# Kernel optimization log

Hardware: AMD Instinct MI355X
Metric: run time of the kernel (lower is better)

## Reference

```python
import jax, jax.numpy as jnp
import numpy as np
import math


def setup_inputs() -> dict:
    key = jax.random.key(0)
    ks = jax.random.split(key, 10)
    B, N, C, heads = 16, 1024, 256, 8
    nW = 4
    ANGLE_BINS = 5
    inner = C  # dim_head*heads == dim
    return {
        "x": jax.random.normal(ks[0], (B, N, C), jnp.float32),
        "mask": jax.random.normal(ks[1], (nW, N, N), jnp.float32),
        "affine_matrix": jax.random.normal(ks[2], (B, 2, 3), jnp.float32),
        "Wq": jax.random.normal(ks[3], (C, inner), jnp.float32) * (C ** -0.5),
        "bq": jnp.zeros((inner,), jnp.float32),
        "Wkv": jax.random.normal(ks[4], (C, 2 * inner), jnp.float32) * (C ** -0.5),
        "bkv": jnp.zeros((2 * inner,), jnp.float32),
        "Wp": jax.random.normal(ks[5], (C, C), jnp.float32) * (C ** -0.5),
        "bp": jnp.zeros((C,), jnp.float32),
        "angle_table": jnp.ones((ANGLE_BINS, heads), jnp.float32),
        "H": 32,
        "W": 32,
    }


def reference(x, mask, affine_matrix, Wq, bq, Wkv, bkv, Wp, bp, angle_table, H, W):
    B, N, C = x.shape
    heads = angle_table.shape[1]
    hd = C // heads
    scale = hd ** -0.5

    # qkv projections (torch Linear -> x @ W + b with W stored as (in, out))
    q = (x @ Wq + bq).reshape(B, N, heads, hd).transpose(0, 2, 1, 3)      # (B,h,N,d)
    kv = (x @ Wkv + bkv).reshape(B, N, 2, heads, hd).transpose(2, 0, 3, 1, 4)
    k, v = kv[0], kv[1]                                                    # (B,h,N,d)

    attn = jnp.einsum('bhqd,bhkd->bhqk', q * scale, k)                     # (B,h,N,N)

    # angle bias: per-query multiplicative bias in (1,2)
    grid_y, grid_x = jnp.meshgrid(jnp.arange(H), jnp.arange(W), indexing='ij')
    coords = jnp.stack([grid_x.reshape(-1), grid_y.reshape(-1)], -1).astype(jnp.float32)  # (N,2)
    center = jnp.array([W / 2.0, H / 2.0], jnp.float32)
    ego = jnp.einsum('bij,j->bi', affine_matrix[:, :2, :2], center) + affine_matrix[:, :2, 2]  # (B,2)
    rel = coords[None, :, :] - ego[:, None, :]                             # (B,N,2)
    ang = jnp.arctan2(rel[..., 1], rel[..., 0])
    bins = (((ang + math.pi) / (2.0 * math.pi)) * (angle_table.shape[0] - 1)).astype(jnp.int32)
    bias = 1.0 + jax.nn.sigmoid(angle_table[bins])                         # (B,N,h)
    attn = attn * bias.transpose(0, 2, 1)[..., None]                       # broadcast over keys

    # additive window mask then softmax
    nW = mask.shape[0]
    attn = attn.reshape(B // nW, nW, heads, N, N) + mask[None, :, None]
    attn = jax.nn.softmax(attn.reshape(B, heads, N, N), axis=-1)

    out = jnp.einsum('bhqk,bhkd->bhqd', attn, v).transpose(0, 2, 1, 3).reshape(B, N, C)
    return out @ Wp + bp
```

## Files before the change

### kernel.cpp

```cpp
#include <hip/hip_runtime.h>
#include <hip/hip_bf16.h>
#include <math.h>

#define BB 16
#define NTOK 1024
#define CDIM 256
#define HEADS 8
#define HD 32
#define LOG2E 1.4426950408889634f
#define PSHIFT 18.0f

typedef __attribute__((ext_vector_type(8))) _Float16 half8;
typedef __attribute__((ext_vector_type(8))) unsigned short u16x8;
typedef __attribute__((ext_vector_type(4))) unsigned int u32x4;
typedef __attribute__((ext_vector_type(2))) unsigned int u32x2;
typedef __attribute__((ext_vector_type(4))) float f32x4;

__device__ __forceinline__ unsigned short f2h(float f) {
  _Float16 h = (_Float16)f;
  return __builtin_bit_cast(unsigned short, h);
}
__device__ __forceinline__ half8 ldh8(const unsigned short* p) {
  return *reinterpret_cast<const half8*>(p);
}
__device__ __forceinline__ void gl_lds16(const unsigned short* g,
                                         unsigned short* l) {
  __builtin_amdgcn_global_load_lds(
      (const __attribute__((address_space(1))) unsigned int*)g,
      (__attribute__((address_space(3))) unsigned int*)l, 16, 0, 0);
}

__global__ __launch_bounds__(256) void cvt_x(const float* __restrict__ X,
                                             unsigned short* __restrict__ x16) {
  size_t base = ((size_t)blockIdx.x * 256 + threadIdx.x) * 8;
  float4 a = *(const float4*)(X + base);
  float4 b = *(const float4*)(X + base + 4);
  u16x8 o = {f2h(a.x), f2h(a.y), f2h(a.z), f2h(a.w),
             f2h(b.x), f2h(b.y), f2h(b.z), f2h(b.w)};
  *(u16x8*)(x16 + base) = o;
}

__global__ __launch_bounds__(256) void cvt_w(
    const float* __restrict__ Wq, const float* __restrict__ Wkv,
    const float* __restrict__ Wp, unsigned short* __restrict__ wt16,
    unsigned short* __restrict__ wp16) {
  int idx = blockIdx.x * 256 + threadIdx.x;
  float val; size_t dst; bool isp = false;
  if (idx < 65536) {
    int k = idx >> 8, n = idx & 255;
    val = Wq[idx]; dst = (size_t)n * 256 + k;
  } else if (idx < 196608) {
    int i2 = idx - 65536;
    int k = i2 >> 9, n2 = i2 & 511;
    val = Wkv[i2]; dst = (size_t)(256 + n2) * 256 + k;
  } else {
    int i3 = idx - 196608;
    int k = i3 >> 8, n = i3 & 255;
    val = Wp[i3]; dst = (size_t)n * 256 + k; isp = true;
  }
  unsigned short h = f2h(val);
  if (isp) wp16[dst] = h; else wt16[dst] = h;
}

__global__ __launch_bounds__(256) void bias_kernel(
    const float* __restrict__ affine, const float* __restrict__ atab,
    float* __restrict__ bias) {
  int idx = blockIdx.x * 256 + threadIdx.x;
  if (idx >= BB * NTOK) return;
  int b = idx >> 10, n = idx & (NTOK - 1);
  float cx = (float)(n & 31);
  float cy = (float)(n >> 5);
  const float* A = affine + b * 6;
  float egx = fmaf(A[0], 16.f, fmaf(A[1], 16.f, A[2]));
  float egy = fmaf(A[3], 16.f, fmaf(A[4], 16.f, A[5]));
  float ang = atan2f(cy - egy, cx - egx);
  float t = (ang + 3.14159265358979323846f) *
            (1.f / (2.f * 3.14159265358979323846f)) * 4.f;
  int bin = (int)t;
  bin = bin < 0 ? 0 : (bin > 4 ? 4 : bin);
  for (int h = 0; h < HEADS; ++h) {
    float a = atab[bin * HEADS + h];
    float s = 1.f / (1.f + __expf(-a));
    bias[((size_t)b * HEADS + h) * NTOK + n] = 1.f + s;
  }
}

__global__ __launch_bounds__(256) void mask_prepF(const float* __restrict__ m,
                                                  float* __restrict__ mF) {
  int idx = blockIdx.x * 256 + threadIdx.x;
  int b4 = idx >> 18;
  int rem = idx & 262143;
  int q = rem >> 8;
  int k = (rem & 255) * 4;
  float4 v = *(const float4*)(m + ((size_t)b4 * NTOK + q) * NTOK + k);
  float4 o = {fmaf(v.x, LOG2E, -PSHIFT), fmaf(v.y, LOG2E, -PSHIFT),
              fmaf(v.z, LOG2E, -PSHIFT), fmaf(v.w, LOG2E, -PSHIFT)};
  int kt = k >> 6, f = (k >> 4) & 3, ins = k & 15;
  size_t dst = ((size_t)((b4 * 16 + kt) * 4 + f)) * 16384 + q * 16 + ins;
  *(float4*)(mF + dst) = o;
}

__global__ __launch_bounds__(512, 4) void gemm_qkv16(
    const unsigned short* __restrict__ x16, const unsigned short* __restrict__ wt16,
    const float* __restrict__ bq, const float* __restrict__ bkv,
    const float* __restrict__ bias, unsigned short* __restrict__ q16,
    unsigned short* __restrict__ k16, unsigned short* __restrict__ vt16) {
  __shared__ __align__(16) unsigned short SM[16384];
  unsigned short* Xs = SM;
  unsigned short* Ws = SM + 8192;
  int tid = threadIdx.x;
  int w = tid >> 6, l = tid & 63;
  int row16 = l & 15, grp = l >> 4;
  int bid = blockIdx.x;
  int xcd = bid & 7, local = bid >> 3;
  int jb = local % 6, mb = xcd * 16 + local / 6;
  int j0 = jb * 128, m0 = mb * 128;
  int wm = w >> 1, wn = w & 1;

  auto stg = [&](int nb, int kt) {
    int k0s = kt * 32;
    int row = w * 16 + (l >> 2);
    int ge = (((l & 3) * 16) ^ ((row & 3) << 4)) >> 1;
    gl_lds16(x16 + (size_t)(m0 + row) * 256 + k0s + ge, Xs + nb * 4096 + w * 512);
    gl_lds16(wt16 + (size_t)(j0 + row) * 256 + k0s + ge, Ws + nb * 4096 + w * 512);
  };
  auto off16 = [&](int row, int g) {
    return row * 32 + ((((g * 16) ^ ((row & 3) << 4))) >> 1);
  };

  stg(0, 0);
  __syncthreads();

  f32x4 acc[2][4];
#pragma unroll
  for (int i = 0; i < 2; ++i)
#pragma unroll
    for (int c = 0; c < 4; ++c) acc[i][c] = (f32x4){0.f, 0.f, 0.f, 0.f};

  for (int kt = 0; kt < 8; ++kt) {
    int cur = kt & 1;
    if (kt < 7) stg(cur ^ 1, kt + 1);
    half8 a0 = ldh8(Xs + cur * 4096 + off16(wm * 32 + row16, grp));
    half8 a1 = ldh8(Xs + cur * 4096 + off16(wm * 32 + 16 + row16, grp));
#pragma unroll
    for (int c = 0; c < 4; ++c) {
      half8 bh = ldh8(Ws + cur * 4096 + off16(wn * 64 + c * 16 + row16, grp));
      acc[0][c] = __builtin_amdgcn_mfma_f32_16x16x32_f16(a0, bh, acc[0][c], 0, 0, 0);
      acc[1][c] = __builtin_amdgcn_mfma_f32_16x16x32_f16(a1, bh, acc[1][c], 0, 0, 0);
    }
    __syncthreads();
  }

  const float scaleq = 0.17677669529663687f * LOG2E;
  int half_mine = wm >> 1;
  for (int half = 0; half < 2; ++half) {
    if (half_mine == half) {
#pragma unroll
      for (int i = 0; i < 2; ++i) {
#pragma unroll
        for (int c = 0; c < 4; ++c) {
          int col = wn * 64 + c * 16 + row16;
          int jg = j0 + col;
#pragma unroll
          for (int r = 0; r < 4; ++r) {
            int rowl = (wm & 1) * 32 + i * 16 + grp * 4 + r;
            int m = m0 + half * 64 + rowl;
            int b = m >> 10, n = m & (NTOK - 1);
            float val = acc[i][c][r];
            unsigned short o;
            if (jb < 2)
              o = f2h((val + bq[jg]) * scaleq *
                      bias[((size_t)b * HEADS + (jg >> 5)) * NTOK + n]);
            else
              o = f2h(val + bkv[jg - CDIM]);
            SM[rowl * 136 + col] = o;
          }
        }
      }
    }
    __syncthreads();
    if (jb < 4) {
#pragma unroll
      for (int it = 0; it < 2; ++it) {
        int lin = it * 512 + tid;
        int rowb = lin >> 4, oct = lin & 15;
        u16x8 v = *(const u16x8*)&SM[rowb * 136 + oct * 8];
        int m = m0 + half * 64 + rowb;
        int b = m >> 10, n = m & (NTOK - 1);
        int jg = j0 + oct * 8;
        unsigned short* dst; int h, d;
        if (jb < 2) { h = jg >> 5; d = jg & 31; dst = q16; }
        else { int c2 = jg - CDIM; h = c2 >> 5; d = c2 & 31; dst = k16; }
        *(u16x8*)(dst + (((size_t)b * HEADS + h) * NTOK + n) * HD + d) = v;
      }
    } else {
#pragma unroll
      for (int it = 0; it < 2; ++it) {
        int lin = it * 512 + tid;
        int noct = lin >> 7, jl = lin & 127;
        u16x8 v;
#pragma unroll
        for (int e = 0; e < 8; ++e) v[e] = SM[(noct * 8 + e) * 136 + jl];
        int c3 = j0 + jl - 2 * CDIM;
        int h = c3 >> 5, d = c3 & 31;
        int n0 = m0 + half * 64 + noct * 8;
        int b = n0 >> 10, nn = n0 & (NTOK - 1);
        *(u16x8*)(vt16 + (((size_t)b * HEADS + h) * HD + d) * NTOK + nn) = v;
      }
    }
    __syncthreads();
  }
}

__global__ __launch_bounds__(512, 8) void attn16(
    const unsigned short* __restrict__ q16, const unsigned short* __restrict__ k16,
    const unsigned short* __restrict__ vt16, const float* __restrict__ maskF,
    unsigned short* __restrict__ ao16) {
  __shared__ __align__(16) unsigned short KT[2][64 * 32];
  __shared__ __align__(16) unsigned short VT[2][32 * 64];
  __shared__ __align__(16) unsigned Pp[8][16][20];

  int tid = threadIdx.x;
  int w = tid >> 6, l = tid & 63;
  int row16 = l & 15, grp = l >> 4;
  int bid = blockIdx.x;
  int swz = (bid & 7) * 128 + (bid >> 3);
  int qt = swz & 7, h = (swz >> 3) & 7, b = swz >> 6;
  int q0 = qt * 128;
  int bh = b * HEADS + h;

  size_t qidx = (((size_t)bh * NTOK) + q0 + w * 16 + row16) * HD + grp * 8;
  half8 bq16 = ldh8(q16 + qidx);

  const float* mFb = maskF + (size_t)(b & 3) * 64 * 16384 +
                     (q0 + w * 16 + row16) * 16 + grp * 4;

  f32x4 accd[2];
  accd[0] = (f32x4){0.f, 0.f, 0.f, 0.f};
  accd[1] = (f32x4){0.f, 0.f, 0.f, 0.f};
  float lsum = 0.f;

  auto stage = [&](int nbuf, int kt2) {
    int k0n = kt2 * 64;
    if (w < 4) {
      int kl = w * 16 + (l >> 2);
      int gd = (((l & 3) * 16) ^ ((kl & 3) << 4)) >> 1;
      gl_lds16(k16 + (((size_t)bh * NTOK) + k0n + kl) * HD + gd,
               &KT[nbuf][w * 16 * 32]);
    } else {
      int sub = w - 4;
      int dl = sub * 8 + (l >> 3);
      int gk = (((l & 7) * 16) ^ ((dl & 7) << 4)) >> 1;
      gl_lds16(vt16 + ((size_t)bh * HD + dl) * NTOK + k0n + gk,
               &VT[nbuf][sub * 8 * 64]);
    }
  };

  stage(0, 0);
  __syncthreads();

  for (int kt = 0; kt < 16; ++kt) {
    int cur = kt & 1;
    if (kt < 15) stage(cur ^ 1, kt + 1);

    f32x4 mC[4];
#pragma unroll
    for (int f = 0; f < 4; ++f)
      mC[f] = *(const f32x4*)(mFb + (size_t)(kt * 4 + f) * 16384);

#pragma unroll
    for (int hf = 0; hf < 2; ++hf) {
      f32x4 s[2];
#pragma unroll
      for (int fp = 0; fp < 2; ++fp) {
        int f = hf * 2 + fp;
        int kl = f * 16 + row16;
        int cb = (grp * 16) ^ ((kl & 3) << 4);
        half8 kf = ldh8(&KT[cur][kl * 32 + (cb >> 1)]);
        s[fp] = __builtin_amdgcn_mfma_f32_16x16x32_f16(kf, bq16, mC[f], 0, 0, 0);
      }
#pragma unroll
      for (int fp = 0; fp < 2; ++fp) {
        float p0 = __builtin_amdgcn_exp2f(s[fp][0]);
        float p1 = __builtin_amdgcn_exp2f(s[fp][1]);
        float p2 = __builtin_amdgcn_exp2f(s[fp][2]);
        float p3 = __builtin_amdgcn_exp2f(s[fp][3]);
        lsum += (p0 + p1) + (p2 + p3);
        unsigned pk01 =
            __builtin_bit_cast(unsigned, __builtin_amdgcn_cvt_pkrtz(p0, p1));
        unsigned pk23 =
            __builtin_bit_cast(unsigned, __builtin_amdgcn_cvt_pkrtz(p2, p3));
        *(u32x2*)&Pp[w][row16][fp * 8 + grp * 2] = (u32x2){pk01, pk23};
      }
      half8 pa =
          __builtin_bit_cast(half8, *(const u32x4*)&Pp[w][row16][grp * 4]);
#pragma unroll
      for (int df = 0; df < 2; ++df) {
        int dl = df * 16 + row16;
        int cb = (hf * 64 + grp * 16) ^ ((dl & 7) << 4);
        half8 v = ldh8(&VT[cur][dl * 64 + (cb >> 1)]);
        accd[df] = __builtin_amdgcn_mfma_f32_16x16x32_f16(pa, v, accd[df], 0, 0, 0);
      }
    }
    __syncthreads();
  }

  lsum += __shfl_xor(lsum, 16);
  lsum += __shfl_xor(lsum, 32);
#pragma unroll
  for (int r = 0; r < 4; ++r) {
    float lr = __shfl(lsum, grp * 4 + r, 16);
    float inv = 1.f / lr;
    int qrow = q0 + w * 16 + grp * 4 + r;
    size_t obase = ((size_t)b * NTOK + qrow) * CDIM + h * HD;
    ao16[obase + row16] = f2h(accd[0][r] * inv);
    ao16[obase + 16 + row16] = f2h(accd[1][r] * inv);
  }
}

__global__ __launch_bounds__(512, 4) void gemm_out16(
    const unsigned short* __restrict__ a16, const unsigned short* __restrict__ wp16,
    const float* __restrict__ bp, float* __restrict__ out) {
  __shared__ __align__(16) unsigned short SM[16384];
  unsigned short* Xs = SM;
  unsigned short* Ws = SM + 8192;
  int tid = threadIdx.x;
  int w = tid >> 6, l = tid & 63;
  int row16 = l & 15, grp = l >> 4;
  int bid = blockIdx.x;
  int xcd = bid & 7, local = bid >> 3;
  int jb = local & 1, mb = xcd * 16 + (local >> 1);
  int j0 = jb * 128, m0 = mb * 128;
  int wm = w >> 1, wn = w & 1;

  auto stg = [&](int nb, int kt) {
    int k0s = kt * 32;
    int row = w * 16 + (l >> 2);
    int ge = (((l & 3) * 16) ^ ((row & 3) << 4)) >> 1;
    gl_lds16(a16 + (size_t)(m0 + row) * 256 + k0s + ge, Xs + nb * 4096 + w * 512);
    gl_lds16(wp16 + (size_t)(j0 + row) * 256 + k0s + ge, Ws + nb * 4096 + w * 512);
  };
  auto off16 = [&](int row, int g) {
    return row * 32 + ((((g * 16) ^ ((row & 3) << 4))) >> 1);
  };

  stg(0, 0);
  __syncthreads();

  f32x4 acc[2][4];
#pragma unroll
  for (int i = 0; i < 2; ++i)
#pragma unroll
    for (int c = 0; c < 4; ++c) acc[i][c] = (f32x4){0.f, 0.f, 0.f, 0.f};

  for (int kt = 0; kt < 8; ++kt) {
    int cur = kt & 1;
    if (kt < 7) stg(cur ^ 1, kt + 1);
    half8 a0 = ldh8(Xs + cur * 4096 + off16(wm * 32 + row16, grp));
    half8 a1 = ldh8(Xs + cur * 4096 + off16(wm * 32 + 16 + row16, grp));
#pragma unroll
    for (int c = 0; c < 4; ++c) {
      half8 bh = ldh8(Ws + cur * 4096 + off16(wn * 64 + c * 16 + row16, grp));
      acc[0][c] = __builtin_amdgcn_mfma_f32_16x16x32_f16(a0, bh, acc[0][c], 0, 0, 0);
      acc[1][c] = __builtin_amdgcn_mfma_f32_16x16x32_f16(a1, bh, acc[1][c], 0, 0, 0);
    }
    __syncthreads();
  }

#pragma unroll
  for (int i = 0; i < 2; ++i) {
    int ng = m0 + wm * 32 + i * 16 + grp * 4;
#pragma unroll
    for (int c = 0; c < 4; ++c) {
      int jg = j0 + wn * 64 + c * 16 + row16;
      float bias = bp[jg];
#pragma unroll
      for (int r = 0; r < 4; ++r) {
        out[(size_t)(ng + r) * CDIM + jg] = acc[i][c][r] + bias;
      }
    }
  }
}

extern "C" void kernel_launch(void* const* d_in, const int* in_sizes, int n_in,
                              void* d_out, int out_size, void* d_ws,
                              size_t ws_size, hipStream_t stream) {
  const float* x = (const float*)d_in[0];
  const float* mask = (const float*)d_in[1];
  const float* affine = (const float*)d_in[2];
  const float* Wq = (const float*)d_in[3];
  const float* bq = (const float*)d_in[4];
  const float* Wkv = (const float*)d_in[5];
  const float* bkv = (const float*)d_in[6];
  const float* Wp = (const float*)d_in[7];
  const float* bp = (const float*)d_in[8];
  const float* atab = (const float*)d_in[9];
  float* out = (float*)d_out;

  const size_t bhnd = (size_t)BB * HEADS * NTOK * HD;
  unsigned short* q16 = (unsigned short*)d_ws;
  unsigned short* k16 = q16 + bhnd;
  unsigned short* vt16 = k16 + bhnd;
  unsigned short* x16 = vt16 + bhnd;
  unsigned short* wt16 = x16 + bhnd;
  unsigned short* wp16 = wt16 + 768 * 256;
  float* bias = (float*)(wp16 + 256 * 256);
  float* maskF = bias + (size_t)BB * HEADS * NTOK;

  cvt_x<<<2048, 256, 0, stream>>>(x, x16);
  cvt_w<<<1024, 256, 0, stream>>>(Wq, Wkv, Wp, wt16, wp16);
  bias_kernel<<<64, 256, 0, stream>>>(affine, atab, bias);
  mask_prepF<<<4096, 256, 0, stream>>>(mask, maskF);
  gemm_qkv16<<<768, 512, 0, stream>>>(x16, wt16, bq, bkv, bias, q16, k16, vt16);
  attn16<<<1024, 512, 0, stream>>>(q16, k16, vt16, maskF, x16);
  gemm_out16<<<256, 512, 0, stream>>>(x16, wp16, bp, out);
}
```

Before: 98.00 us.

## Triple-buffer LDS staging with one barrier per step and new XOR swizzle

```diff
diff --git a/kernel.cpp b/kernel.cpp
--- a/kernel.cpp
+++ b/kernel.cpp
@@ -100,14 +100,20 @@
   *(float4*)(mF + dst) = o;
 }
 
+__device__ __forceinline__ int off16(int row, int g) {
+  int R = row >> 1;
+  int p = (((row & 1) << 2) | g) ^ (R & 7);
+  return R * 64 + p * 8;
+}
+
 __global__ __launch_bounds__(512, 4) void gemm_qkv16(
     const unsigned short* __restrict__ x16, const unsigned short* __restrict__ wt16,
     const float* __restrict__ bq, const float* __restrict__ bkv,
     const float* __restrict__ bias, unsigned short* __restrict__ q16,
     unsigned short* __restrict__ k16, unsigned short* __restrict__ vt16) {
-  __shared__ __align__(16) unsigned short SM[16384];
+  __shared__ __align__(16) unsigned short SM[24576];
   unsigned short* Xs = SM;
-  unsigned short* Ws = SM + 8192;
+  unsigned short* Ws = SM + 12288;
   int tid = threadIdx.x;
   int w = tid >> 6, l = tid & 63;
   int row16 = l & 15, grp = l >> 4;
@@ -118,18 +124,17 @@
   int wm = w >> 1, wn = w & 1;
 
   auto stg = [&](int nb, int kt) {
-    int k0s = kt * 32;
-    int row = w * 16 + (l >> 2);
-    int ge = (((l & 3) * 16) ^ ((row & 3) << 4)) >> 1;
-    gl_lds16(x16 + (size_t)(m0 + row) * 256 + k0s + ge, Xs + nb * 4096 + w * 512);
-    gl_lds16(wt16 + (size_t)(j0 + row) * 256 + k0s + ge, Ws + nb * 4096 + w * 512);
+    int k0s = (kt & 7) * 32;
+    int R = w * 8 + (l >> 3);
+    int q = (l & 7) ^ (R & 7);
+    int row = 2 * R + (q >> 2);
+    int ce = (q & 3) * 8;
+    gl_lds16(x16 + (size_t)(m0 + row) * 256 + k0s + ce, Xs + nb * 4096 + w * 512);
+    gl_lds16(wt16 + (size_t)(j0 + row) * 256 + k0s + ce, Ws + nb * 4096 + w * 512);
   };
-  auto off16 = [&](int row, int g) {
-    return row * 32 + ((((g * 16) ^ ((row & 3) << 4))) >> 1);
-  };
 
   stg(0, 0);
-  __syncthreads();
+  stg(1, 1);
 
   f32x4 acc[2][4];
 #pragma unroll
@@ -138,8 +143,10 @@
     for (int c = 0; c < 4; ++c) acc[i][c] = (f32x4){0.f, 0.f, 0.f, 0.f};
 
   for (int kt = 0; kt < 8; ++kt) {
-    int cur = kt & 1;
-    if (kt < 7) stg(cur ^ 1, kt + 1);
+    int cur = kt % 3;
+    asm volatile("s_waitcnt vmcnt(2)" ::: "memory");
+    __builtin_amdgcn_s_barrier();
+    stg((kt + 2) % 3, kt + 2);
     half8 a0 = ldh8(Xs + cur * 4096 + off16(wm * 32 + row16, grp));
     half8 a1 = ldh8(Xs + cur * 4096 + off16(wm * 32 + 16 + row16, grp));
 #pragma unroll
@@ -148,8 +155,9 @@
       acc[0][c] = __builtin_amdgcn_mfma_f32_16x16x32_f16(a0, bh, acc[0][c], 0, 0, 0);
       acc[1][c] = __builtin_amdgcn_mfma_f32_16x16x32_f16(a1, bh, acc[1][c], 0, 0, 0);
     }
-    __syncthreads();
-  }
+  }
+  asm volatile("s_waitcnt vmcnt(0)" ::: "memory");
+  __syncthreads();
 
   const float scaleq = 0.17677669529663687f * LOG2E;
   int half_mine = wm >> 1;
@@ -216,8 +224,8 @@
     const unsigned short* __restrict__ q16, const unsigned short* __restrict__ k16,
     const unsigned short* __restrict__ vt16, const float* __restrict__ maskF,
     unsigned short* __restrict__ ao16) {
-  __shared__ __align__(16) unsigned short KT[2][64 * 32];
-  __shared__ __align__(16) unsigned short VT[2][32 * 64];
+  __shared__ __align__(16) unsigned short KT[3][2048];
+  __shared__ __align__(16) unsigned short VT[3][2048];
   __shared__ __align__(16) unsigned Pp[8][16][20];
 
   int tid = threadIdx.x;
@@ -241,32 +249,37 @@
   float lsum = 0.f;
 
   auto stage = [&](int nbuf, int kt2) {
-    int k0n = kt2 * 64;
+    int k0n = (kt2 & 15) * 64;
     if (w < 4) {
-      int kl = w * 16 + (l >> 2);
-      int gd = (((l & 3) * 16) ^ ((kl & 3) << 4)) >> 1;
-      gl_lds16(k16 + (((size_t)bh * NTOK) + k0n + kl) * HD + gd,
-               &KT[nbuf][w * 16 * 32]);
+      int R = w * 8 + (l >> 3);
+      int q = (l & 7) ^ (R & 7);
+      int row = 2 * R + (q >> 2);
+      int col = (q & 3) * 8;
+      gl_lds16(k16 + (((size_t)bh * NTOK) + k0n + row) * HD + col,
+               &KT[nbuf][w * 512]);
     } else {
       int sub = w - 4;
       int dl = sub * 8 + (l >> 3);
       int gk = (((l & 7) * 16) ^ ((dl & 7) << 4)) >> 1;
       gl_lds16(vt16 + ((size_t)bh * HD + dl) * NTOK + k0n + gk,
-               &VT[nbuf][sub * 8 * 64]);
+               &VT[nbuf][sub * 512]);
     }
   };
 
   stage(0, 0);
-  __syncthreads();
+  stage(1, 1);
 
   for (int kt = 0; kt < 16; ++kt) {
-    int cur = kt & 1;
-    if (kt < 15) stage(cur ^ 1, kt + 1);
+    int cur = kt % 3;
+    asm volatile("s_waitcnt vmcnt(1)" ::: "memory");
+    __builtin_amdgcn_s_barrier();
 
     f32x4 mC[4];
 #pragma unroll
     for (int f = 0; f < 4; ++f)
       mC[f] = *(const f32x4*)(mFb + (size_t)(kt * 4 + f) * 16384);
+    __builtin_amdgcn_sched_barrier(0);
+    stage((kt + 2) % 3, kt + 2);
 
 #pragma unroll
     for (int hf = 0; hf < 2; ++hf) {
@@ -275,8 +288,7 @@
       for (int fp = 0; fp < 2; ++fp) {
         int f = hf * 2 + fp;
         int kl = f * 16 + row16;
-        int cb = (grp * 16) ^ ((kl & 3) << 4);
-        half8 kf = ldh8(&KT[cur][kl * 32 + (cb >> 1)]);
+        half8 kf = ldh8(&KT[cur][off16(kl, grp)]);
         s[fp] = __builtin_amdgcn_mfma_f32_16x16x32_f16(kf, bq16, mC[f], 0, 0, 0);
       }
 #pragma unroll
@@ -302,8 +314,8 @@
         accd[df] = __builtin_amdgcn_mfma_f32_16x16x32_f16(pa, v, accd[df], 0, 0, 0);
       }
     }
-    __syncthreads();
-  }
+  }
+  asm volatile("s_waitcnt vmcnt(0)" ::: "memory");
 
   lsum += __shfl_xor(lsum, 16);
   lsum += __shfl_xor(lsum, 32);
@@ -321,9 +333,9 @@
 __global__ __launch_bounds__(512, 4) void gemm_out16(
     const unsigned short* __restrict__ a16, const unsigned short* __restrict__ wp16,
     const float* __restrict__ bp, float* __restrict__ out) {
-  __shared__ __align__(16) unsigned short SM[16384];
+  __shared__ __align__(16) unsigned short SM[24576];
   unsigned short* Xs = SM;
-  unsigned short* Ws = SM + 8192;
+  unsigned short* Ws = SM + 12288;
   int tid = threadIdx.x;
   int w = tid >> 6, l = tid & 63;
   int row16 = l & 15, grp = l >> 4;
@@ -334,18 +346,17 @@
   int wm = w >> 1, wn = w & 1;
 
   auto stg = [&](int nb, int kt) {
-    int k0s = kt * 32;
-    int row = w * 16 + (l >> 2);
-    int ge = (((l & 3) * 16) ^ ((row & 3) << 4)) >> 1;
-    gl_lds16(a16 + (size_t)(m0 + row) * 256 + k0s + ge, Xs + nb * 4096 + w * 512);
-    gl_lds16(wp16 + (size_t)(j0 + row) * 256 + k0s + ge, Ws + nb * 4096 + w * 512);
+    int k0s = (kt & 7) * 32;
+    int R = w * 8 + (l >> 3);
+    int q = (l & 7) ^ (R & 7);
+    int row = 2 * R + (q >> 2);
+    int ce = (q & 3) * 8;
+    gl_lds16(a16 + (size_t)(m0 + row) * 256 + k0s + ce, Xs + nb * 4096 + w * 512);
+    gl_lds16(wp16 + (size_t)(j0 + row) * 256 + k0s + ce, Ws + nb * 4096 + w * 512);
   };
-  auto off16 = [&](int row, int g) {
-    return row * 32 + ((((g * 16) ^ ((row & 3) << 4))) >> 1);
-  };
 
   stg(0, 0);
-  __syncthreads();
+  stg(1, 1);
 
   f32x4 acc[2][4];
 #pragma unroll
@@ -354,8 +365,10 @@
     for (int c = 0; c < 4; ++c) acc[i][c] = (f32x4){0.f, 0.f, 0.f, 0.f};
 
   for (int kt = 0; kt < 8; ++kt) {
-    int cur = kt & 1;
-    if (kt < 7) stg(cur ^ 1, kt + 1);
+    int cur = kt % 3;
+    asm volatile("s_waitcnt vmcnt(2)" ::: "memory");
+    __builtin_amdgcn_s_barrier();
+    stg((kt + 2) % 3, kt + 2);
     half8 a0 = ldh8(Xs + cur * 4096 + off16(wm * 32 + row16, grp));
     half8 a1 = ldh8(Xs + cur * 4096 + off16(wm * 32 + 16 + row16, grp));
 #pragma unroll
@@ -364,8 +377,8 @@
       acc[0][c] = __builtin_amdgcn_mfma_f32_16x16x32_f16(a0, bh, acc[0][c], 0, 0, 0);
       acc[1][c] = __builtin_amdgcn_mfma_f32_16x16x32_f16(a1, bh, acc[1][c], 0, 0, 0);
     }
-    __syncthreads();
-  }
+  }
+  asm volatile("s_waitcnt vmcnt(0)" ::: "memory");
 
 #pragma unroll
   for (int i = 0; i < 2; ++i) {
```

New measurement: 100.3 us. 1.02x slower.

## Permute key order so softmax probabilities stay in registers without LDS round-trip

Applied to the files above, without the earlier changes.

```diff
diff --git a/kernel.cpp b/kernel.cpp
--- a/kernel.cpp
+++ b/kernel.cpp
@@ -13,7 +13,6 @@
 typedef __attribute__((ext_vector_type(8))) _Float16 half8;
 typedef __attribute__((ext_vector_type(8))) unsigned short u16x8;
 typedef __attribute__((ext_vector_type(4))) unsigned int u32x4;
-typedef __attribute__((ext_vector_type(2))) unsigned int u32x2;
 typedef __attribute__((ext_vector_type(4))) float f32x4;
 
 __device__ __forceinline__ unsigned short f2h(float f) {
@@ -95,9 +94,12 @@
   float4 v = *(const float4*)(m + ((size_t)b4 * NTOK + q) * NTOK + k);
   float4 o = {fmaf(v.x, LOG2E, -PSHIFT), fmaf(v.y, LOG2E, -PSHIFT),
               fmaf(v.z, LOG2E, -PSHIFT), fmaf(v.w, LOG2E, -PSHIFT)};
-  int kt = k >> 6, f = (k >> 4) & 3, ins = k & 15;
-  size_t dst = ((size_t)((b4 * 16 + kt) * 4 + f)) * 16384 + q * 16 + ins;
-  *(float4*)(mF + dst) = o;
+  int kt = k >> 6, hf = (k >> 5) & 1, a = (k & 31) >> 2;
+  size_t base = ((size_t)((b4 * 16 + kt) * 4 + hf * 2)) * 16384 + q * 16 + a * 2;
+  float2 e = {o.x, o.z};
+  float2 d = {o.y, o.w};
+  *(float2*)(mF + base) = e;
+  *(float2*)(mF + base + 16384) = d;
 }
 
 __global__ __launch_bounds__(512, 4) void gemm_qkv16(
@@ -216,9 +218,8 @@
     const unsigned short* __restrict__ q16, const unsigned short* __restrict__ k16,
     const unsigned short* __restrict__ vt16, const float* __restrict__ maskF,
     unsigned short* __restrict__ ao16) {
-  __shared__ __align__(16) unsigned short KT[2][64 * 32];
-  __shared__ __align__(16) unsigned short VT[2][32 * 64];
-  __shared__ __align__(16) unsigned Pp[8][16][20];
+  __shared__ __align__(16) unsigned short KT[2][2048];
+  __shared__ __align__(16) unsigned short VT[2][2048];
 
   int tid = threadIdx.x;
   int w = tid >> 6, l = tid & 63;
@@ -243,9 +244,10 @@
   auto stage = [&](int nbuf, int kt2) {
     int k0n = kt2 * 64;
     if (w < 4) {
-      int kl = w * 16 + (l >> 2);
-      int gd = (((l & 3) * 16) ^ ((kl & 3) << 4)) >> 1;
-      gl_lds16(k16 + (((size_t)bh * NTOK) + k0n + kl) * HD + gd,
+      int r = w * 16 + (l >> 2);
+      int key = ((r >> 5) << 5) + 2 * (r & 15) + ((r >> 4) & 1);
+      int gd = (((l & 3) * 16) ^ ((r & 3) << 4)) >> 1;
+      gl_lds16(k16 + (((size_t)bh * NTOK) + k0n + key) * HD + gd,
                &KT[nbuf][w * 16 * 32]);
     } else {
       int sub = w - 4;
@@ -277,23 +279,23 @@
         int kl = f * 16 + row16;
         int cb = (grp * 16) ^ ((kl & 3) << 4);
         half8 kf = ldh8(&KT[cur][kl * 32 + (cb >> 1)]);
-        s[fp] = __builtin_amdgcn_mfma_f32_16x16x32_f16(kf, bq16, mC[f], 0, 0, 0);
-      }
-#pragma unroll
-      for (int fp = 0; fp < 2; ++fp) {
-        float p0 = __builtin_amdgcn_exp2f(s[fp][0]);
-        float p1 = __builtin_amdgcn_exp2f(s[fp][1]);
-        float p2 = __builtin_amdgcn_exp2f(s[fp][2]);
-        float p3 = __builtin_amdgcn_exp2f(s[fp][3]);
-        lsum += (p0 + p1) + (p2 + p3);
-        unsigned pk01 =
-            __builtin_bit_cast(unsigned, __builtin_amdgcn_cvt_pkrtz(p0, p1));
-        unsigned pk23 =
-            __builtin_bit_cast(unsigned, __builtin_amdgcn_cvt_pkrtz(p2, p3));
-        *(u32x2*)&Pp[w][row16][fp * 8 + grp * 2] = (u32x2){pk01, pk23};
-      }
-      half8 pa =
-          __builtin_bit_cast(half8, *(const u32x4*)&Pp[w][row16][grp * 4]);
+        s[fp] = __builtin_amdgcn_mfma_f32_16x16x32_f16(kf, bq16,
+                                                       mC[f], 0, 0, 0);
+      }
+      f32x4 e0, e1;
+#pragma unroll
+      for (int r = 0; r < 4; ++r) {
+        e0[r] = __builtin_amdgcn_exp2f(s[0][r]);
+        e1[r] = __builtin_amdgcn_exp2f(s[1][r]);
+      }
+      lsum += ((e0[0] + e1[0]) + (e0[1] + e1[1])) +
+              ((e0[2] + e1[2]) + (e0[3] + e1[3]));
+      u32x4 pk;
+#pragma unroll
+      for (int r = 0; r < 4; ++r)
+        pk[r] = __builtin_bit_cast(unsigned,
+                                   __builtin_amdgcn_cvt_pkrtz(e0[r], e1[r]));
+      half8 pa = __builtin_bit_cast(half8, pk);
 #pragma unroll
       for (int df = 0; df < 2; ++df) {
         int dl = df * 16 + row16;
```

New measurement: 99.11 us. About the same (+1.1%).
